# Performance work log

Hardware: AMD Instinct MI355X
Metric: run time of the kernel (lower is better)

Reference implementation:

```python
import jax, jax.numpy as jnp
import numpy as np

NUM_WIRES = 4
NUM_LAYERS = 2


def _apply_ry(state, w, theta):
    # state: (N, 2,2,2,2); theta: scalar or (N,)
    st = jnp.moveaxis(state, 1 + w, -1)
    c = jnp.cos(theta / 2)
    s = jnp.sin(theta / 2)
    # broadcast (N,) -> (N,1,1,1) against st[...,k] of shape (N,2,2,2)
    c = c.reshape(c.shape + (1,) * (st.ndim - 1 - c.ndim))
    s = s.reshape(s.shape + (1,) * (st.ndim - 1 - s.ndim))
    a0, a1 = st[..., 0], st[..., 1]
    st = jnp.stack([c * a0 - s * a1, s * a0 + c * a1], axis=-1)
    return jnp.moveaxis(st, -1, 1 + w)


def _apply_rz(state, w, theta):
    st = jnp.moveaxis(state, 1 + w, -1)
    p = jnp.exp(-0.5j * theta)  # phase on |0>; conj on |1>
    st = jnp.stack([st[..., 0] * p, st[..., 1] * jnp.conj(p)], axis=-1)
    return jnp.moveaxis(st, -1, 1 + w)


def _apply_cnot(state, cw, tw):
    st = jnp.moveaxis(state, (1 + cw, 1 + tw), (-2, -1))
    st = jnp.stack([st[..., 0, :], st[..., 1, ::-1]], axis=-2)
    return jnp.moveaxis(st, (-2, -1), (1 + cw, 1 + tw))


def _circuit(angles, params):
    # angles: (N, 4) RY input angles; params: (L, 4, 3)
    N = angles.shape[0]
    state = jnp.zeros((N, 2, 2, 2, 2), jnp.complex64).at[:, 0, 0, 0, 0].set(1.0)
    for i in range(NUM_WIRES):
        state = _apply_ry(state, i, angles[:, i])
    for l in range(NUM_LAYERS):
        for i in range(NUM_WIRES):
            state = _apply_ry(state, i, params[l, i, 0])
        for i in range(NUM_WIRES - 1):
            state = _apply_cnot(state, i, i + 1)
        for i in range(NUM_WIRES):
            state = _apply_ry(state, i, params[l, i, 1])
        for i in range(NUM_WIRES - 1):
            state = _apply_cnot(state, i + 1, i)
        for i in range(NUM_WIRES):
            state = _apply_rz(state, i, params[l, i, 2])
    probs = state.real ** 2 + state.imag ** 2  # (N,2,2,2,2)
    zs = []
    for i in range(NUM_WIRES):
        axes = tuple(a for a in range(1, 1 + NUM_WIRES) if a != 1 + i)
        marg = probs.sum(axis=axes)  # (N,2)
        zs.append(marg[:, 0] - marg[:, 1])
    return jnp.stack(zs, axis=1)  # (N,4)


def setup_inputs() -> dict:
    key = jax.random.key(0)
    kx, kp = jax.random.split(key)
    x = jax.random.normal(kx, (512, 28, 28), dtype=jnp.float32)
    params = jax.random.normal(kp, (NUM_LAYERS, NUM_WIRES, 3), dtype=jnp.float32)
    return {"x": x, "params": params}


def reference(x, params):
    B = x.shape[0]
    # extract non-overlapping 2x2 patches, row-major over (r, c), patch order
    # [x[r,c], x[r,c+1], x[r+1,c], x[r+1,c+1]] matching .view(batch, -1)
    patches = x.reshape(B, 14, 2, 14, 2).transpose(0, 1, 3, 2, 4).reshape(B, 196, 4)
    # per-patch-location scalar normalization over all batch*4 elements (ddof=1 std)
    n = B * 4
    m = patches.mean(axis=(0, 2), keepdims=True)
    sd = jnp.sqrt(((patches - m) ** 2).sum(axis=(0, 2), keepdims=True) / (n - 1))
    angles = (patches - m) / (sd + 1e-8) * jnp.pi
    z = _circuit(angles.reshape(B * 196, 4), params)  # (B*196, 4)
    return z.reshape(B, 196 * 4).astype(jnp.float32)
```

## Files before the change

### kernel.cpp

```cpp
#include <hip/hip_runtime.h>
#include <math.h>

#define BATCH   512
#define NPATCH  196


template <int MASK>
__device__ __forceinline__ void ry_real(float* s, float c, float sn) {
    #pragma unroll
    for (int i = 0; i < 16; ++i) {
        if (!(i & MASK)) {
            const int j = i | MASK;
            float a0 = s[i], a1 = s[j];
            s[i] = c * a0 - sn * a1;
            s[j] = sn * a0 + c * a1;
        }
    }
}

template <int MASK>
__device__ __forceinline__ void ry_cplx(float* sr, float* si, float c, float sn) {
    #pragma unroll
    for (int i = 0; i < 16; ++i) {
        if (!(i & MASK)) {
            const int j = i | MASK;
            float a0 = sr[i], a1 = sr[j];
            sr[i] = c * a0 - sn * a1;
            sr[j] = sn * a0 + c * a1;
            float b0 = si[i], b1 = si[j];
            si[i] = c * b0 - sn * b1;
            si[j] = sn * b0 + c * b1;
        }
    }
}

template <int CMASK, int TMASK>
__device__ __forceinline__ void cnot_real(float* s) {
    #pragma unroll
    for (int i = 0; i < 16; ++i) {
        if ((i & CMASK) && !(i & TMASK)) {
            const int j = i | TMASK;
            float t = s[i]; s[i] = s[j]; s[j] = t;
        }
    }
}

template <int CMASK, int TMASK>
__device__ __forceinline__ void cnot_cplx(float* sr, float* si) {
    #pragma unroll
    for (int i = 0; i < 16; ++i) {
        if ((i & CMASK) && !(i & TMASK)) {
            const int j = i | TMASK;
            float t;
            t = sr[i]; sr[i] = sr[j]; sr[j] = t;
            t = si[i]; si[i] = si[j]; si[j] = t;
        }
    }
}

__global__ __launch_bounds__(512) void fused_kernel(const float* __restrict__ x,
                                                    const float* __restrict__ params,
                                                    float* __restrict__ out) {
    __shared__ float s_ryc[16], s_rys[16];
    __shared__ float s_pc[16], s_ps[16];
    __shared__ float s_sum[8], s_sq[8];
    __shared__ float s_m, s_invh;

    const int p = blockIdx.x;
    const int r = p / 14, c = p - r * 14;
    const int t = threadIdx.x;

    if (t < 16) {
        const int l = t >> 3, set = (t >> 2) & 1, w = t & 3;
        float sn, cs;
        __sincosf(0.5f * params[l * 12 + w * 3 + set], &sn, &cs);
        s_ryc[t] = cs;
        s_rys[t] = sn;
    } else if (t < 32) {
        const int i = t - 16;
        const float h0 = 0.5f * params[0 * 3 + 2];
        const float h1 = 0.5f * params[1 * 3 + 2];
        const float h2 = 0.5f * params[2 * 3 + 2];
        const float h3 = 0.5f * params[3 * 3 + 2];
        const float alpha = ((i & 8) ? h0 : -h0) + ((i & 4) ? h1 : -h1)
                          + ((i & 2) ? h2 : -h2) + ((i & 1) ? h3 : -h3);
        float sn, cs;
        __sincosf(alpha, &sn, &cs);
        s_pc[i] = cs;
        s_ps[i] = sn;
    }

    const float* base = x + t * 784 + (2 * r) * 28 + 2 * c;
    const float2 a01 = *(const float2*)base;
    const float2 a23 = *(const float2*)(base + 28);

    float sum = a01.x + a01.y + a23.x + a23.y;
    float sq  = a01.x * a01.x + a01.y * a01.y + a23.x * a23.x + a23.y * a23.y;
    #pragma unroll
    for (int off = 32; off; off >>= 1) {
        sum += __shfl_down(sum, off, 64);
        sq  += __shfl_down(sq,  off, 64);
    }
    const int wave = t >> 6, lane = t & 63;
    if (lane == 0) { s_sum[wave] = sum; s_sq[wave] = sq; }
    __syncthreads();
    if (t == 0) {
        float S = 0.f, Q = 0.f;
        #pragma unroll
        for (int w = 0; w < 8; ++w) { S += s_sum[w]; Q += s_sq[w]; }
        const float n = (float)(BATCH * 4);
        float m   = S / n;
        float var = (Q - S * S / n) / (n - 1.0f);
        float sd  = sqrtf(fmaxf(var, 0.f));
        s_m    = m;
        s_invh = 0.5f * 3.14159265358979323846f / (sd + 1e-8f);
    }
    __syncthreads();

    const float m    = s_m;
    const float invh = s_invh;

    float c0, s0, c1, s1, c2, s2, c3, s3;
    __sincosf((a01.x - m) * invh, &s0, &c0);
    __sincosf((a01.y - m) * invh, &s1, &c1);
    __sincosf((a23.x - m) * invh, &s2, &c2);
    __sincosf((a23.y - m) * invh, &s3, &c3);

    float sr[16];
    {
        const float cc01 = c0 * c1, cs01 = c0 * s1, sc01 = s0 * c1, ss01 = s0 * s1;
        const float cc23 = c2 * c3, cs23 = c2 * s3, sc23 = s2 * c3, ss23 = s2 * s3;
        #pragma unroll
        for (int i = 0; i < 16; ++i) {
            const float hi = (i & 8) ? ((i & 4) ? ss01 : sc01) : ((i & 4) ? cs01 : cc01);
            const float lo = (i & 2) ? ((i & 1) ? ss23 : sc23) : ((i & 1) ? cs23 : cc23);
            sr[i] = hi * lo;
        }
    }

    ry_real<8>(sr, s_ryc[0], s_rys[0]);
    ry_real<4>(sr, s_ryc[1], s_rys[1]);
    ry_real<2>(sr, s_ryc[2], s_rys[2]);
    ry_real<1>(sr, s_ryc[3], s_rys[3]);
    cnot_real<8, 4>(sr);
    cnot_real<4, 2>(sr);
    cnot_real<2, 1>(sr);
    ry_real<8>(sr, s_ryc[4], s_rys[4]);
    ry_real<4>(sr, s_ryc[5], s_rys[5]);
    ry_real<2>(sr, s_ryc[6], s_rys[6]);
    ry_real<1>(sr, s_ryc[7], s_rys[7]);
    cnot_real<4, 8>(sr);
    cnot_real<2, 4>(sr);
    cnot_real<1, 2>(sr);

    float si[16];
    #pragma unroll
    for (int i = 0; i < 16; ++i) {
        si[i] = sr[i] * s_ps[i];
        sr[i] = sr[i] * s_pc[i];
    }

    ry_cplx<8>(sr, si, s_ryc[8],  s_rys[8]);
    ry_cplx<4>(sr, si, s_ryc[9],  s_rys[9]);
    ry_cplx<2>(sr, si, s_ryc[10], s_rys[10]);
    ry_cplx<1>(sr, si, s_ryc[11], s_rys[11]);
    cnot_cplx<8, 4>(sr, si);
    cnot_cplx<4, 2>(sr, si);
    cnot_cplx<2, 1>(sr, si);
    ry_cplx<8>(sr, si, s_ryc[12], s_rys[12]);
    ry_cplx<4>(sr, si, s_ryc[13], s_rys[13]);
    ry_cplx<2>(sr, si, s_ryc[14], s_rys[14]);
    ry_cplx<1>(sr, si, s_ryc[15], s_rys[15]);
    cnot_cplx<4, 8>(sr, si);
    cnot_cplx<2, 4>(sr, si);
    cnot_cplx<1, 2>(sr, si);

    float pr[16];
    #pragma unroll
    for (int i = 0; i < 16; ++i) pr[i] = sr[i] * sr[i] + si[i] * si[i];

    float a[8], z3 = 0.f;
    #pragma unroll
    for (int k = 0; k < 8; ++k) {
        a[k] = pr[2 * k] + pr[2 * k + 1];
        z3  += pr[2 * k] - pr[2 * k + 1];
    }
    float b[4], z2 = 0.f;
    #pragma unroll
    for (int k = 0; k < 4; ++k) {
        b[k] = a[2 * k] + a[2 * k + 1];
        z2  += a[2 * k] - a[2 * k + 1];
    }
    float g2[2], z1 = 0.f;
    #pragma unroll
    for (int k = 0; k < 2; ++k) {
        g2[k] = b[2 * k] + b[2 * k + 1];
        z1   += b[2 * k] - b[2 * k + 1];
    }
    const float z0 = g2[0] - g2[1];

    *(float4*)(out + t * (NPATCH * 4) + p * 4) = make_float4(z0, z1, z2, z3);
}

extern "C" void kernel_launch(void* const* d_in, const int* in_sizes, int n_in,
                              void* d_out, int out_size, void* d_ws, size_t ws_size,
                              hipStream_t stream) {
    (void)in_sizes; (void)n_in; (void)d_ws; (void)ws_size; (void)out_size;
    const float* x      = (const float*)d_in[0];
    const float* params = (const float*)d_in[1];
    float*       out    = (float*)d_out;

    fused_kernel<<<NPATCH, 512, 0, stream>>>(x, params, out);
}
```

Before: 61.83 us.

## Split into patch-transpose kernel and circuit kernel for coalesced loads

Adds a pre-pass kernel that stages each image in shared memory and writes 2x2 patches into a workspace laid out patch-major, batch-minor. The circuit kernel then reads one contiguous float4 per thread instead of strided float2 loads spaced 784 floats apart. It also drops the second barrier by having every thread compute the mean and std from shared partial sums. The cost is an extra kernel launch and a full round trip of the input through global workspace memory.

```diff
diff --git a/kernel.cpp b/kernel.cpp
--- a/kernel.cpp
+++ b/kernel.cpp
@@ -4,6 +4,26 @@
 #define BATCH   512
 #define NPATCH  196
 
+__global__ __launch_bounds__(256) void patch_kernel(const float* __restrict__ x,
+                                                    float4* __restrict__ ws) {
+    __shared__ float lx[784];
+    const int b = blockIdx.x;
+    const int t = threadIdx.x;
+    if (t < 196) {
+        ((float4*)lx)[t] = ((const float4*)(x + b * 784))[t];
+    }
+    __syncthreads();
+    if (t < 196) {
+        const int r = t / 14, c = t - r * 14;
+        const float* row = lx + (2 * r) * 28 + 2 * c;
+        float4 v;
+        v.x = row[0];
+        v.y = row[1];
+        v.z = row[28];
+        v.w = row[29];
+        ws[t * BATCH + b] = v;
+    }
+}
 
 template <int MASK>
 __device__ __forceinline__ void ry_real(float* s, float c, float sn) {
@@ -58,17 +78,17 @@
     }
 }
 
-__global__ __launch_bounds__(512) void fused_kernel(const float* __restrict__ x,
-                                                    const float* __restrict__ params,
-                                                    float* __restrict__ out) {
+__global__ __launch_bounds__(512) void circuit_kernel(const float4* __restrict__ ws,
+                                                      const float* __restrict__ params,
+                                                      float* __restrict__ out) {
     __shared__ float s_ryc[16], s_rys[16];
     __shared__ float s_pc[16], s_ps[16];
     __shared__ float s_sum[8], s_sq[8];
-    __shared__ float s_m, s_invh;
 
     const int p = blockIdx.x;
-    const int r = p / 14, c = p - r * 14;
     const int t = threadIdx.x;
+
+    const float4 v = ws[p * BATCH + t];
 
     if (t < 16) {
         const int l = t >> 3, set = (t >> 2) & 1, w = t & 3;
@@ -78,10 +98,10 @@
         s_rys[t] = sn;
     } else if (t < 32) {
         const int i = t - 16;
-        const float h0 = 0.5f * params[0 * 3 + 2];
-        const float h1 = 0.5f * params[1 * 3 + 2];
-        const float h2 = 0.5f * params[2 * 3 + 2];
-        const float h3 = 0.5f * params[3 * 3 + 2];
+        const float h0 = 0.5f * params[2];
+        const float h1 = 0.5f * params[5];
+        const float h2 = 0.5f * params[8];
+        const float h3 = 0.5f * params[11];
         const float alpha = ((i & 8) ? h0 : -h0) + ((i & 4) ? h1 : -h1)
                           + ((i & 2) ? h2 : -h2) + ((i & 1) ? h3 : -h3);
         float sn, cs;
@@ -90,12 +110,8 @@
         s_ps[i] = sn;
     }
 
-    const float* base = x + t * 784 + (2 * r) * 28 + 2 * c;
-    const float2 a01 = *(const float2*)base;
-    const float2 a23 = *(const float2*)(base + 28);
-
-    float sum = a01.x + a01.y + a23.x + a23.y;
-    float sq  = a01.x * a01.x + a01.y * a01.y + a23.x * a23.x + a23.y * a23.y;
+    float sum = v.x + v.y + v.z + v.w;
+    float sq  = v.x * v.x + v.y * v.y + v.z * v.z + v.w * v.w;
     #pragma unroll
     for (int off = 32; off; off >>= 1) {
         sum += __shfl_down(sum, off, 64);
@@ -104,27 +120,21 @@
     const int wave = t >> 6, lane = t & 63;
     if (lane == 0) { s_sum[wave] = sum; s_sq[wave] = sq; }
     __syncthreads();
-    if (t == 0) {
-        float S = 0.f, Q = 0.f;
-        #pragma unroll
-        for (int w = 0; w < 8; ++w) { S += s_sum[w]; Q += s_sq[w]; }
-        const float n = (float)(BATCH * 4);
-        float m   = S / n;
-        float var = (Q - S * S / n) / (n - 1.0f);
-        float sd  = sqrtf(fmaxf(var, 0.f));
-        s_m    = m;
-        s_invh = 0.5f * 3.14159265358979323846f / (sd + 1e-8f);
-    }
-    __syncthreads();
-
-    const float m    = s_m;
-    const float invh = s_invh;
+
+    float S = 0.f, Q = 0.f;
+    #pragma unroll
+    for (int w = 0; w < 8; ++w) { S += s_sum[w]; Q += s_sq[w]; }
+    const float n   = (float)(BATCH * 4);
+    const float m   = S / n;
+    const float var = (Q - S * S / n) / (n - 1.0f);
+    const float sd  = sqrtf(fmaxf(var, 0.f));
+    const float invh = 0.5f * 3.14159265358979323846f / (sd + 1e-8f);
 
     float c0, s0, c1, s1, c2, s2, c3, s3;
-    __sincosf((a01.x - m) * invh, &s0, &c0);
-    __sincosf((a01.y - m) * invh, &s1, &c1);
-    __sincosf((a23.x - m) * invh, &s2, &c2);
-    __sincosf((a23.y - m) * invh, &s3, &c3);
+    __sincosf((v.x - m) * invh, &s0, &c0);
+    __sincosf((v.y - m) * invh, &s1, &c1);
+    __sincosf((v.z - m) * invh, &s2, &c2);
+    __sincosf((v.w - m) * invh, &s3, &c3);
 
     float sr[16];
     {
@@ -185,17 +195,17 @@
         a[k] = pr[2 * k] + pr[2 * k + 1];
         z3  += pr[2 * k] - pr[2 * k + 1];
     }
-    float b[4], z2 = 0.f;
+    float b4[4], z2 = 0.f;
     #pragma unroll
     for (int k = 0; k < 4; ++k) {
-        b[k] = a[2 * k] + a[2 * k + 1];
-        z2  += a[2 * k] - a[2 * k + 1];
+        b4[k] = a[2 * k] + a[2 * k + 1];
+        z2   += a[2 * k] - a[2 * k + 1];
     }
     float g2[2], z1 = 0.f;
     #pragma unroll
     for (int k = 0; k < 2; ++k) {
-        g2[k] = b[2 * k] + b[2 * k + 1];
-        z1   += b[2 * k] - b[2 * k + 1];
+        g2[k] = b4[2 * k] + b4[2 * k + 1];
+        z1   += b4[2 * k] - b4[2 * k + 1];
     }
     const float z0 = g2[0] - g2[1];
 
@@ -205,10 +215,12 @@
 extern "C" void kernel_launch(void* const* d_in, const int* in_sizes, int n_in,
                               void* d_out, int out_size, void* d_ws, size_t ws_size,
                               hipStream_t stream) {
-    (void)in_sizes; (void)n_in; (void)d_ws; (void)ws_size; (void)out_size;
+    (void)in_sizes; (void)n_in; (void)ws_size; (void)out_size;
     const float* x      = (const float*)d_in[0];
     const float* params = (const float*)d_in[1];
     float*       out    = (float*)d_out;
-
-    fused_kernel<<<NPATCH, 512, 0, stream>>>(x, params, out);
-}
+    float4*      ws     = (float4*)d_ws;
+
+    patch_kernel<<<BATCH, 256, 0, stream>>>(x, ws);
+    circuit_kernel<<<NPATCH, 512, 0, stream>>>(ws, params, out);
+}
```

After: 63.54 us. +2.8%, slower.

## Fold first RY layer into input angles and drop second block barrier

Applied to the files above, without the earlier changes.

Merges the first layer of RY rotations into the input encoding angles, since consecutive RY gates on the same wire add their angles. This removes four real RY passes per thread. Every thread now computes the mean and std from the per-wave partial sums itself, which drops the single-thread finalize step and one __syncthreads. The global loads are also issued before the parameter setup so their latency can overlap it. The cost is redundant per-thread reduction arithmetic and a few more shared reads.

```diff
diff --git a/kernel.cpp b/kernel.cpp
--- a/kernel.cpp
+++ b/kernel.cpp
@@ -3,7 +3,6 @@
 
 #define BATCH   512
 #define NPATCH  196
-
 
 template <int MASK>
 __device__ __forceinline__ void ry_real(float* s, float c, float sn) {
@@ -63,12 +62,16 @@
                                                     float* __restrict__ out) {
     __shared__ float s_ryc[16], s_rys[16];
     __shared__ float s_pc[16], s_ps[16];
+    __shared__ float s_half[4];
     __shared__ float s_sum[8], s_sq[8];
-    __shared__ float s_m, s_invh;
 
     const int p = blockIdx.x;
     const int r = p / 14, c = p - r * 14;
     const int t = threadIdx.x;
+
+    const float* base = x + t * 784 + (2 * r) * 28 + 2 * c;
+    const float2 a01 = *(const float2*)base;
+    const float2 a23 = *(const float2*)(base + 28);
 
     if (t < 16) {
         const int l = t >> 3, set = (t >> 2) & 1, w = t & 3;
@@ -78,21 +81,19 @@
         s_rys[t] = sn;
     } else if (t < 32) {
         const int i = t - 16;
-        const float h0 = 0.5f * params[0 * 3 + 2];
-        const float h1 = 0.5f * params[1 * 3 + 2];
-        const float h2 = 0.5f * params[2 * 3 + 2];
-        const float h3 = 0.5f * params[3 * 3 + 2];
+        const float h0 = 0.5f * params[2];
+        const float h1 = 0.5f * params[5];
+        const float h2 = 0.5f * params[8];
+        const float h3 = 0.5f * params[11];
         const float alpha = ((i & 8) ? h0 : -h0) + ((i & 4) ? h1 : -h1)
                           + ((i & 2) ? h2 : -h2) + ((i & 1) ? h3 : -h3);
         float sn, cs;
         __sincosf(alpha, &sn, &cs);
         s_pc[i] = cs;
         s_ps[i] = sn;
-    }
-
-    const float* base = x + t * 784 + (2 * r) * 28 + 2 * c;
-    const float2 a01 = *(const float2*)base;
-    const float2 a23 = *(const float2*)(base + 28);
+    } else if (t < 36) {
+        s_half[t - 32] = 0.5f * params[(t - 32) * 3];
+    }
 
     float sum = a01.x + a01.y + a23.x + a23.y;
     float sq  = a01.x * a01.x + a01.y * a01.y + a23.x * a23.x + a23.y * a23.y;
@@ -104,27 +105,21 @@
     const int wave = t >> 6, lane = t & 63;
     if (lane == 0) { s_sum[wave] = sum; s_sq[wave] = sq; }
     __syncthreads();
-    if (t == 0) {
-        float S = 0.f, Q = 0.f;
-        #pragma unroll
-        for (int w = 0; w < 8; ++w) { S += s_sum[w]; Q += s_sq[w]; }
-        const float n = (float)(BATCH * 4);
-        float m   = S / n;
-        float var = (Q - S * S / n) / (n - 1.0f);
-        float sd  = sqrtf(fmaxf(var, 0.f));
-        s_m    = m;
-        s_invh = 0.5f * 3.14159265358979323846f / (sd + 1e-8f);
-    }
-    __syncthreads();
-
-    const float m    = s_m;
-    const float invh = s_invh;
+
+    float S = 0.f, Q = 0.f;
+    #pragma unroll
+    for (int w = 0; w < 8; ++w) { S += s_sum[w]; Q += s_sq[w]; }
+    const float n   = (float)(BATCH * 4);
+    const float m   = S / n;
+    const float var = (Q - S * S / n) / (n - 1.0f);
+    const float sd  = sqrtf(fmaxf(var, 0.f));
+    const float invh = 0.5f * 3.14159265358979323846f / (sd + 1e-8f);
 
     float c0, s0, c1, s1, c2, s2, c3, s3;
-    __sincosf((a01.x - m) * invh, &s0, &c0);
-    __sincosf((a01.y - m) * invh, &s1, &c1);
-    __sincosf((a23.x - m) * invh, &s2, &c2);
-    __sincosf((a23.y - m) * invh, &s3, &c3);
+    __sincosf((a01.x - m) * invh + s_half[0], &s0, &c0);
+    __sincosf((a01.y - m) * invh + s_half[1], &s1, &c1);
+    __sincosf((a23.x - m) * invh + s_half[2], &s2, &c2);
+    __sincosf((a23.y - m) * invh + s_half[3], &s3, &c3);
 
     float sr[16];
     {
@@ -138,10 +133,6 @@
         }
     }
 
-    ry_real<8>(sr, s_ryc[0], s_rys[0]);
-    ry_real<4>(sr, s_ryc[1], s_rys[1]);
-    ry_real<2>(sr, s_ryc[2], s_rys[2]);
-    ry_real<1>(sr, s_ryc[3], s_rys[3]);
     cnot_real<8, 4>(sr);
     cnot_real<4, 2>(sr);
     cnot_real<2, 1>(sr);
@@ -185,17 +176,17 @@
         a[k] = pr[2 * k] + pr[2 * k + 1];
         z3  += pr[2 * k] - pr[2 * k + 1];
     }
-    float b[4], z2 = 0.f;
+    float b4[4], z2 = 0.f;
     #pragma unroll
     for (int k = 0; k < 4; ++k) {
-        b[k] = a[2 * k] + a[2 * k + 1];
-        z2  += a[2 * k] - a[2 * k + 1];
+        b4[k] = a[2 * k] + a[2 * k + 1];
+        z2   += a[2 * k] - a[2 * k + 1];
     }
     float g2[2], z1 = 0.f;
     #pragma unroll
     for (int k = 0; k < 2; ++k) {
-        g2[k] = b[2 * k] + b[2 * k + 1];
-        z1   += b[2 * k] - b[2 * k + 1];
+        g2[k] = b4[2 * k] + b4[2 * k + 1];
+        z1   += b4[2 * k] - b4[2 * k + 1];
     }
     const float z0 = g2[0] - g2[1];
 
```

New measurement: 60.71 us. No clear change (-1.8%).
